# Kernel tuning notes

Hardware: AMD Instinct MI355X
Metric: run time of the kernel (lower is better)

## Reference

```python
import jax, jax.numpy as jnp
import numpy as np

B, S, D, H = 2, 2048, 1024, 16
DH = D // H  # dim_per_head = 64


def setup_inputs() -> dict:
    key = jax.random.key(0)
    ks = jax.random.split(key, 12)
    scale = 1.0 / np.sqrt(D)
    inp = {
        "key": jax.random.normal(ks[0], (B, S, D), jnp.float32),
        "value": jax.random.normal(ks[1], (B, S, D), jnp.float32),
        "query": jax.random.normal(ks[2], (B, S, D), jnp.float32),
        "mask": jax.random.randint(ks[3], (B, S, S), 0, 2) == 1,
        "Wq": jax.random.normal(ks[4], (D, D), jnp.float32) * scale,
        "bq": jnp.zeros((D,), jnp.float32),
        "Wk": jax.random.normal(ks[5], (D, D), jnp.float32) * scale,
        "bk": jnp.zeros((D,), jnp.float32),
        "Wv": jax.random.normal(ks[6], (D, D), jnp.float32) * scale,
        "bv": jnp.zeros((D,), jnp.float32),
        "Wo": jax.random.normal(ks[7], (D, D), jnp.float32) * scale,
        "bo": jnp.zeros((D,), jnp.float32),
    }
    return inp


def reference(key, value, query, mask, Wq, bq, Wk, bk, Wv, bv, Wo, bo):
    b, s, d = query.shape
    dh = d // H

    def split_heads(x):  # [b, s, d] -> [b, H, s, dh]
        return x.reshape(b, -1, H, dh).transpose(0, 2, 1, 3)

    q = split_heads(query @ Wq + bq) / jnp.sqrt(jnp.float32(dh))
    k = split_heads(key @ Wk + bk)
    v = split_heads(value @ Wv + bv)

    scores = jnp.einsum("bhqd,bhkd->bhqk", q, k)  # [b, H, s, s]
    scores = jnp.where(mask[:, None, :, :], jnp.float32(-1e18), scores)
    attn = jax.nn.softmax(scores, axis=-1)  # dropout is identity in eval
    ctx = jnp.einsum("bhqk,bhkd->bhqd", attn, v)
    ctx = ctx.transpose(0, 2, 1, 3).reshape(b, s, d)
    return ctx @ Wo + bo
```

## Files before the change

kernel.cpp:

```cpp
#include <hip/hip_runtime.h>
#include <hip/hip_bf16.h>

#define BATCH  2
#define SEQ    2048
#define DMODEL 1024
#define NHEAD  16
#define DHEAD  64
#define NTOK   (BATCH * SEQ)

using f32x4 = __attribute__((ext_vector_type(4))) float;
using s16x4 = __attribute__((ext_vector_type(4))) short;
using s16x8 = __attribute__((ext_vector_type(8))) short;

__device__ __forceinline__ short f2bf(float f) {
  __hip_bfloat16 h = __float2bfloat16(f);
  return *(short*)&h;
}

__device__ __forceinline__ void gload_lds16(const short* g, short* l) {
  __builtin_amdgcn_global_load_lds(
      (const __attribute__((address_space(1))) void*)g,
      (__attribute__((address_space(3))) void*)l, 16, 0, 0);
}

__global__ __launch_bounds__(256) void wtrans_kernel(
    const float* __restrict__ Wq, const float* __restrict__ Wk,
    const float* __restrict__ Wv, const float* __restrict__ Wo,
    short* __restrict__ Wt) {
  __shared__ short tile[64][72];
  const float* W = blockIdx.z == 0 ? Wq : blockIdx.z == 1 ? Wk
                 : blockIdx.z == 2 ? Wv : Wo;
  short* out = Wt + (size_t)blockIdx.z * DMODEL * DMODEL;
  int k0 = blockIdx.x * 64, n0 = blockIdx.y * 64;
  int t = threadIdx.x;
#pragma unroll
  for (int i = 0; i < 4; ++i) {
    int idx = t + i * 256;
    int row = idx >> 4, c4 = idx & 15;
    f32x4 v = *(const f32x4*)(W + (size_t)(k0 + row) * DMODEL + n0 + c4 * 4);
    s16x4 p;
    p[0] = f2bf(v[0]); p[1] = f2bf(v[1]); p[2] = f2bf(v[2]); p[3] = f2bf(v[3]);
    *(s16x4*)&tile[row][c4 * 4] = p;
  }
  __syncthreads();
#pragma unroll
  for (int i = 0; i < 2; ++i) {
    int idx = t + i * 256;
    int nrow = idx >> 3, c8 = idx & 7;
    s16x8 p;
#pragma unroll
    for (int j = 0; j < 8; ++j) p[j] = tile[c8 * 8 + j][nrow];
    *(s16x8*)(out + (size_t)(n0 + nrow) * DMODEL + k0 + c8 * 8) = p;
  }
}

__global__ __launch_bounds__(256) void mpack_kernel(
    const int* __restrict__ mask, unsigned long long* __restrict__ Mp) {
  const int total_words = BATCH * SEQ * (SEQ / 64);
  int lane = threadIdx.x & 63;
  int wv = blockIdx.x * 4 + (threadIdx.x >> 6);
  int nw = gridDim.x * 4;
  for (int w = wv; w < total_words; w += nw) {
    int mv = mask[(size_t)w * 64 + lane];
    unsigned long long bits = __ballot(mv != 0);
    if (lane == 0) Mp[w] = bits;
  }
}

__global__ __launch_bounds__(256) void proj_qkv_kernel(
    const float* __restrict__ Xq, const float* __restrict__ Xk,
    const float* __restrict__ Xv, const short* __restrict__ Wt,
    const float* __restrict__ bq, const float* __restrict__ bk,
    const float* __restrict__ bv, short* __restrict__ QKV) {
  __shared__ short As[2][128 * 32];
  __shared__ short Bs[2][128 * 32];
  const int sel = blockIdx.z;
  const float* X    = sel == 0 ? Xq : sel == 1 ? Xk : Xv;
  const float* bias = sel == 0 ? bq : sel == 1 ? bk : bv;
  const short* Wsel = Wt + (size_t)sel * DMODEL * DMODEL;
  short* Obuf = QKV + (size_t)sel * ((size_t)BATCH * NHEAD * SEQ * DHEAD);
  const float scale = sel == 0 ? 0.18033688011111793f : 1.0f;

  int m0 = blockIdx.x * 128, n0 = blockIdx.y * 128;
  int t = threadIdx.x, wid = t >> 6, lane = t & 63;
  int lr = lane & 15, lg = lane >> 4;
  int wr = wid >> 1, wc = wid & 1;
  f32x4 acc[4][4] = {};

  const int ar0 = t >> 2, ac0 = (t & 3) << 3;
  const float* Arow0 = X + (size_t)(m0 + ar0) * DMODEL + ac0;
  const float* Arow1 = Arow0 + (size_t)64 * DMODEL;
  const int aofs0 = ar0 * 32 + ac0, aofs1 = aofs0 + 64 * 32;
  const short* Brow0 = Wsel + (size_t)(n0 + ar0) * DMODEL + ac0;
  const short* Brow1 = Brow0 + (size_t)64 * DMODEL;
  const int bofs0 = (t & ~63) << 3, bofs1 = bofs0 + 256 * 8;

  f32x4 a00, a01, a10, a11;
#define LOADA(k0s) {                                                          \
    a00 = *(const f32x4*)(Arow0 + (k0s));                                     \
    a01 = *(const f32x4*)(Arow0 + (k0s) + 4);                                 \
    a10 = *(const f32x4*)(Arow1 + (k0s));                                     \
    a11 = *(const f32x4*)(Arow1 + (k0s) + 4); }
#define STAGEB(bufi, k0s) {                                                   \
    gload_lds16(Brow0 + (k0s), &Bs[bufi][0] + bofs0);                         \
    gload_lds16(Brow1 + (k0s), &Bs[bufi][0] + bofs1); }
#define WRITEA(bufi) {                                                        \
    s16x8 p0, p1;                                                             \
    p0[0]=f2bf(a00[0]); p0[1]=f2bf(a00[1]); p0[2]=f2bf(a00[2]); p0[3]=f2bf(a00[3]); \
    p0[4]=f2bf(a01[0]); p0[5]=f2bf(a01[1]); p0[6]=f2bf(a01[2]); p0[7]=f2bf(a01[3]); \
    p1[0]=f2bf(a10[0]); p1[1]=f2bf(a10[1]); p1[2]=f2bf(a10[2]); p1[3]=f2bf(a10[3]); \
    p1[4]=f2bf(a11[0]); p1[5]=f2bf(a11[1]); p1[6]=f2bf(a11[2]); p1[7]=f2bf(a11[3]); \
    *(s16x8*)(&As[bufi][0] + aofs0) = p0;                                     \
    *(s16x8*)(&As[bufi][0] + aofs1) = p1; }

  LOADA(0); STAGEB(0, 0); WRITEA(0);
  __syncthreads();

  int cur = 0;
  for (int kt = 0; kt < DMODEL / 32; ++kt) {
    if (kt + 1 < DMODEL / 32) {
      LOADA((kt + 1) * 32);
      STAGEB(cur ^ 1, (kt + 1) * 32);
    }
    s16x8 afr[4], bfr[4];
#pragma unroll
    for (int mi = 0; mi < 4; ++mi)
      afr[mi] = *(const s16x8*)(&As[cur][0] + (wr * 64 + mi * 16 + lr) * 32 + lg * 8);
#pragma unroll
    for (int ni = 0; ni < 4; ++ni)
      bfr[ni] = *(const s16x8*)(&Bs[cur][0] + (wc * 64 + ni * 16 + lr) * 32 + lg * 8);
    __builtin_amdgcn_s_setprio(1);
#pragma unroll
    for (int mi = 0; mi < 4; ++mi)
#pragma unroll
      for (int ni = 0; ni < 4; ++ni)
        acc[mi][ni] = __builtin_amdgcn_mfma_f32_16x16x32_bf16(
            afr[mi], bfr[ni], acc[mi][ni], 0, 0, 0);
    __builtin_amdgcn_s_setprio(0);
    if (kt + 1 < DMODEL / 32) WRITEA(cur ^ 1);
    __syncthreads();
    cur ^= 1;
  }
#undef LOADA
#undef STAGEB
#undef WRITEA

  if (sel == 2) {
    int bq_ = m0 >> 11;
    int s0 = (m0 & (SEQ - 1)) + wr * 64 + lg * 4;
#pragma unroll
    for (int mi = 0; mi < 4; ++mi)
#pragma unroll
      for (int ni = 0; ni < 4; ++ni) {
        int n = n0 + wc * 64 + ni * 16 + lr;
        float bv_ = bias[n];
        int h = n >> 6, d = n & 63;
        s16x4 pk;
#pragma unroll
        for (int r = 0; r < 4; ++r) pk[r] = f2bf(acc[mi][ni][r] + bv_);
        *(s16x4*)&Obuf[((size_t)(bq_ * NHEAD + h) * DHEAD + d) * SEQ
                       + s0 + mi * 16] = pk;
      }
  } else {
#pragma unroll
    for (int mi = 0; mi < 4; ++mi)
#pragma unroll
      for (int ni = 0; ni < 4; ++ni) {
        int n = n0 + wc * 64 + ni * 16 + lr;
        float bv_ = bias[n];
        int h = n >> 6, d = n & 63;
#pragma unroll
        for (int r = 0; r < 4; ++r) {
          int m = m0 + wr * 64 + mi * 16 + lg * 4 + r;
          int b = m >> 11, s = m & (SEQ - 1);
          float val = (acc[mi][ni][r] + bv_) * scale;
          Obuf[((size_t)(b * NHEAD + h) * SEQ + s) * DHEAD + d] = f2bf(val);
        }
      }
  }
}

__global__ __launch_bounds__(256) void attn_kernel(
    const short* __restrict__ Qb, const short* __restrict__ Kb,
    const short* __restrict__ VbT, const unsigned long long* __restrict__ Mp,
    short* __restrict__ Ctx) {
  __shared__ short Ks[2][64 * 64];
  __shared__ short Vt[2][64 * 64];
  __shared__ short Ps[4 * 16 * 64];
  int qt = blockIdx.x, bh = blockIdx.y;
  int b = bh >> 4, h = bh & 15;
  int q0 = qt * 64;
  int t = threadIdx.x, wid = t >> 6, lane = t & 63;
  int lr = lane & 15, lg = lane >> 4;
  int lr7 = lr & 7;

  const short* Qrow = Qb + ((size_t)bh * SEQ + q0 + wid * 16 + lr) * DHEAD;
  s16x8 qf[2];
  qf[0] = *(const s16x8*)(Qrow + lg * 8);
  qf[1] = *(const s16x8*)(Qrow + 32 + lg * 8);

  const short* KbB = Kb + (size_t)bh * SEQ * DHEAD;
  const short* VtB = VbT + (size_t)bh * DHEAD * SEQ;

  const int srow = lane >> 3;
  const int schunk = ((lane & 7) ^ srow) * 8;

  float m_run = -1e30f, l_run = 0.f;
  f32x4 o_acc[4] = {};

  const unsigned long long* mrow =
      Mp + ((size_t)b * SEQ + q0 + wid * 16 + lr) * (SEQ / 64);

#define STAGE(bufi, k0s)                                                      \
  {                                                                           \
    _Pragma("unroll")                                                         \
    for (int i = 0; i < 2; ++i) {                                             \
      int rbase = wid * 16 + i * 8;                                           \
      gload_lds16(KbB + (size_t)((k0s) + rbase + srow) * DHEAD + schunk,      \
                  &Ks[bufi][rbase * 64]);                                     \
      gload_lds16(VtB + (size_t)(rbase + srow) * SEQ + (k0s) + schunk,        \
                  &Vt[bufi][rbase * 64]);                                     \
    }                                                                         \
  }

  unsigned long long mw_cur = mrow[0];
  STAGE(0, 0);
  asm volatile("s_waitcnt vmcnt(0)" ::: "memory");
  __syncthreads();

  int cur = 0;
  for (int kt = 0; kt < SEQ / 64; ++kt) {
    unsigned long long mw_next = 0;
    if (kt + 1 < SEQ / 64) {
      STAGE(cur ^ 1, (kt + 1) * 64);
      mw_next = mrow[kt + 1];
    }
    const short* KsC = Ks[cur];
    const short* VtC = Vt[cur];

    f32x4 sfr[4];
    __builtin_amdgcn_s_setprio(1);
#pragma unroll
    for (int nf = 0; nf < 4; ++nf) {
      int row = nf * 16 + lr;
      s16x8 kf0 = *(const s16x8*)&KsC[row * 64 + ((lg ^ lr7) << 3)];
      s16x8 kf1 = *(const s16x8*)&KsC[row * 64 + (((4 + lg) ^ lr7) << 3)];
      f32x4 c = {};
      c = __builtin_amdgcn_mfma_f32_16x16x32_bf16(kf0, qf[0], c, 0, 0, 0);
      c = __builtin_amdgcn_mfma_f32_16x16x32_bf16(kf1, qf[1], c, 0, 0, 0);
      sfr[nf] = c;
    }
    __builtin_amdgcn_s_setprio(0);

    unsigned w0 = (unsigned)(mw_cur >> (lg * 4));
    unsigned w1 = (unsigned)(mw_cur >> (lg * 4 + 32));
#pragma unroll
    for (int nf = 0; nf < 4; ++nf)
#pragma unroll
      for (int r = 0; r < 4; ++r) {
        unsigned bit = (nf < 2) ? (w0 >> (nf * 16 + r)) : (w1 >> ((nf - 2) * 16 + r));
        if (bit & 1u) sfr[nf][r] = -1e30f;
      }
    float tm = fmaxf(fmaxf(fmaxf(sfr[0][0], sfr[0][1]), fmaxf(sfr[0][2], sfr[0][3])),
                     fmaxf(fmaxf(sfr[1][0], sfr[1][1]), fmaxf(sfr[1][2], sfr[1][3])));
    float tm2 = fmaxf(fmaxf(fmaxf(sfr[2][0], sfr[2][1]), fmaxf(sfr[2][2], sfr[2][3])),
                      fmaxf(fmaxf(sfr[3][0], sfr[3][1]), fmaxf(sfr[3][2], sfr[3][3])));
    tm = fmaxf(tm, tm2);
    tm = fmaxf(tm, __shfl_xor(tm, 16, 64));
    tm = fmaxf(tm, __shfl_xor(tm, 32, 64));

    bool small = __all(tm <= m_run + 8.0f);
    if (!small) {
      float mnew = fmaxf(m_run, tm);
      float scl = __builtin_amdgcn_exp2f(m_run - mnew);
      m_run = mnew;
      l_run *= scl;
      float scl_o[4];
#pragma unroll
      for (int r = 0; r < 4; ++r) scl_o[r] = __shfl(scl, lg * 4 + r, 64);
#pragma unroll
      for (int nf = 0; nf < 4; ++nf)
#pragma unroll
        for (int r = 0; r < 4; ++r) o_acc[nf][r] *= scl_o[r];
    }
    float ps4[4];
#pragma unroll
    for (int nf = 0; nf < 4; ++nf) {
#pragma unroll
      for (int r = 0; r < 4; ++r)
        sfr[nf][r] = __builtin_amdgcn_exp2f(sfr[nf][r] - m_run);
      ps4[nf] = (sfr[nf][0] + sfr[nf][1]) + (sfr[nf][2] + sfr[nf][3]);
    }
    float ps = (ps4[0] + ps4[1]) + (ps4[2] + ps4[3]);
    ps += __shfl_xor(ps, 16, 64);
    ps += __shfl_xor(ps, 32, 64);
    l_run += ps;

    int psbase = wid * (16 * 64) + lr * 64;
#pragma unroll
    for (int nf = 0; nf < 4; ++nf) {
      s16x4 pk;
#pragma unroll
      for (int r = 0; r < 4; ++r) pk[r] = f2bf(sfr[nf][r]);
      *(s16x4*)&Ps[psbase + ((((2 * nf + (lg >> 1)) ^ lr7) << 3) | ((lg & 1) << 2))] = pk;
    }
    asm volatile("s_waitcnt lgkmcnt(0)" ::: "memory");
    __builtin_amdgcn_sched_barrier(0);

    __builtin_amdgcn_s_setprio(1);
#pragma unroll
    for (int ks = 0; ks < 2; ++ks) {
      s16x8 pf = *(const s16x8*)&Ps[psbase + (((ks * 4 + lg) ^ lr7) << 3)];
#pragma unroll
      for (int nf = 0; nf < 4; ++nf) {
        int d = nf * 16 + lr;
        s16x8 vf = *(const s16x8*)&VtC[d * 64 + (((ks * 4 + lg) ^ lr7) << 3)];
        o_acc[nf] = __builtin_amdgcn_mfma_f32_16x16x32_bf16(pf, vf, o_acc[nf], 0, 0, 0);
      }
    }
    __builtin_amdgcn_s_setprio(0);

    asm volatile("s_waitcnt vmcnt(0)" ::: "memory");
    __syncthreads();
    cur ^= 1;
    mw_cur = mw_next;
  }
#undef STAGE
  float l_o[4];
#pragma unroll
  for (int r = 0; r < 4; ++r) l_o[r] = __shfl(l_run, lg * 4 + r, 64);
#pragma unroll
  for (int nf = 0; nf < 4; ++nf)
#pragma unroll
    for (int r = 0; r < 4; ++r) {
      int srow_ = q0 + wid * 16 + lg * 4 + r;
      float val = o_acc[nf][r] / l_o[r];
      Ctx[((size_t)b * SEQ + srow_) * DMODEL + h * DHEAD + nf * 16 + lr] = f2bf(val);
    }
}

__global__ __launch_bounds__(256) void proj_out_kernel(
    const short* __restrict__ Ctx, const short* __restrict__ Wot,
    const float* __restrict__ bo, float* __restrict__ Out) {
  __shared__ short As[2][128 * 32];
  __shared__ short Bs[2][128 * 32];
  int m0 = blockIdx.x * 128, n0 = blockIdx.y * 128;
  int t = threadIdx.x, wid = t >> 6, lane = t & 63;
  int lr = lane & 15, lg = lane >> 4;
  int wr = wid >> 1, wc = wid & 1;
  f32x4 acc[4][4] = {};

  const int gr0 = t >> 2, gc0 = (t & 3) << 3;
  const short* Actx0 = Ctx + (size_t)(m0 + gr0) * DMODEL + gc0;
  const short* Actx1 = Actx0 + (size_t)64 * DMODEL;
  const short* Bwo0 = Wot + (size_t)(n0 + gr0) * DMODEL + gc0;
  const short* Bwo1 = Bwo0 + (size_t)64 * DMODEL;
  const int lofs0 = (t & ~63) << 3, lofs1 = lofs0 + 256 * 8;

#define STAGE_PO(bufi, k0s) {                                                 \
    gload_lds16(Actx0 + (k0s), &As[bufi][0] + lofs0);                         \
    gload_lds16(Actx1 + (k0s), &As[bufi][0] + lofs1);                         \
    gload_lds16(Bwo0 + (k0s), &Bs[bufi][0] + lofs0);                          \
    gload_lds16(Bwo1 + (k0s), &Bs[bufi][0] + lofs1); }

  STAGE_PO(0, 0);
  __syncthreads();

  int cur = 0;
  for (int kt = 0; kt < DMODEL / 32; ++kt) {
    if (kt + 1 < DMODEL / 32) STAGE_PO(cur ^ 1, (kt + 1) * 32);
    s16x8 afr[4], bfr[4];
#pragma unroll
    for (int mi = 0; mi < 4; ++mi)
      afr[mi] = *(const s16x8*)(&As[cur][0] + (wr * 64 + mi * 16 + lr) * 32 + lg * 8);
#pragma unroll
    for (int ni = 0; ni < 4; ++ni)
      bfr[ni] = *(const s16x8*)(&Bs[cur][0] + (wc * 64 + ni * 16 + lr) * 32 + lg * 8);
    __builtin_amdgcn_s_setprio(1);
#pragma unroll
    for (int mi = 0; mi < 4; ++mi)
#pragma unroll
      for (int ni = 0; ni < 4; ++ni)
        acc[mi][ni] = __builtin_amdgcn_mfma_f32_16x16x32_bf16(
            afr[mi], bfr[ni], acc[mi][ni], 0, 0, 0);
    __builtin_amdgcn_s_setprio(0);
    __syncthreads();
    cur ^= 1;
  }
#undef STAGE_PO

#pragma unroll
  for (int mi = 0; mi < 4; ++mi)
#pragma unroll
    for (int ni = 0; ni < 4; ++ni) {
      int n = n0 + wc * 64 + ni * 16 + lr;
      float bv_ = bo[n];
#pragma unroll
      for (int r = 0; r < 4; ++r) {
        int m = m0 + wr * 64 + mi * 16 + lg * 4 + r;
        Out[(size_t)m * DMODEL + n] = acc[mi][ni][r] + bv_;
      }
    }
}

extern "C" void kernel_launch(void* const* d_in, const int* in_sizes, int n_in,
                              void* d_out, int out_size, void* d_ws, size_t ws_size,
                              hipStream_t stream) {
  const float* key_in   = (const float*)d_in[0];
  const float* value_in = (const float*)d_in[1];
  const float* query_in = (const float*)d_in[2];
  const int*   mask     = (const int*)d_in[3];
  const float* Wq = (const float*)d_in[4];
  const float* bq = (const float*)d_in[5];
  const float* Wk = (const float*)d_in[6];
  const float* bk = (const float*)d_in[7];
  const float* Wv = (const float*)d_in[8];
  const float* bv = (const float*)d_in[9];
  const float* Wo = (const float*)d_in[10];
  const float* bo = (const float*)d_in[11];
  float* out = (float*)d_out;

  short* ws = (short*)d_ws;
  const size_t WSZ   = (size_t)DMODEL * DMODEL;
  const size_t QKVSZ = (size_t)BATCH * NHEAD * SEQ * DHEAD;
  short* Wt  = ws;
  short* QKV = ws + 4 * WSZ;
  short* Qb  = QKV;
  short* Kb  = QKV + QKVSZ;
  short* VbT = QKV + 2 * QKVSZ;
  short* Ctx = QKV + 3 * QKVSZ;
  unsigned long long* Mp = (unsigned long long*)ws;

  wtrans_kernel<<<dim3(16, 16, 4), 256, 0, stream>>>(Wq, Wk, Wv, Wo, Wt);
  proj_qkv_kernel<<<dim3(32, 8, 3), 256, 0, stream>>>(
      query_in, key_in, value_in, Wt, bq, bk, bv, QKV);
  mpack_kernel<<<dim3(1024), 256, 0, stream>>>(mask, Mp);
  attn_kernel<<<dim3(32, 32), 256, 0, stream>>>(Qb, Kb, VbT, Mp, Ctx);
  proj_out_kernel<<<dim3(32, 8), 256, 0, stream>>>(Ctx, Wt + 3 * WSZ, bo, out);
}
```

Baseline: 190.5 us.

## Pre-cast activations to bf16 and remap grids for XCD-aware block placement

Adds a separate cast kernel that converts query/key/value to bf16 once, so the QKV projection can stage both operands with direct global-to-LDS loads instead of loading fp32 through registers and converting in the inner loop. It also flattens the grids of the projection, attention and output kernels and remaps block indices so consecutive blocks on the same XCD share tiles, aiming for better L2 reuse. The cost is an extra kernel launch plus an extra write and read of the bf16 activations. Ctx now aliases the Xb buffer, which is safe only because the QKV projection finishes before attention writes Ctx.

After: 189.0 us. No clear change (-0.8%).

```diff
diff --git a/kernel.cpp b/kernel.cpp
--- a/kernel.cpp
+++ b/kernel.cpp
@@ -54,6 +54,20 @@
   }
 }
 
+__global__ __launch_bounds__(256) void xcast_kernel(
+    const float* __restrict__ Xq, const float* __restrict__ Xk,
+    const float* __restrict__ Xv, short* __restrict__ Xb) {
+  int sel = blockIdx.y;
+  const float* src = sel == 0 ? Xq : sel == 1 ? Xk : Xv;
+  size_t off = ((size_t)blockIdx.x * 256 + threadIdx.x) * 8;
+  f32x4 v0 = *(const f32x4*)(src + off);
+  f32x4 v1 = *(const f32x4*)(src + off + 4);
+  s16x8 p;
+  p[0] = f2bf(v0[0]); p[1] = f2bf(v0[1]); p[2] = f2bf(v0[2]); p[3] = f2bf(v0[3]);
+  p[4] = f2bf(v1[0]); p[5] = f2bf(v1[1]); p[6] = f2bf(v1[2]); p[7] = f2bf(v1[3]);
+  *(s16x8*)(Xb + (size_t)sel * NTOK * DMODEL + off) = p;
+}
+
 __global__ __launch_bounds__(256) void mpack_kernel(
     const int* __restrict__ mask, unsigned long long* __restrict__ Mp) {
   const int total_words = BATCH * SEQ * (SEQ / 64);
@@ -68,60 +82,48 @@
 }
 
 __global__ __launch_bounds__(256) void proj_qkv_kernel(
-    const float* __restrict__ Xq, const float* __restrict__ Xk,
-    const float* __restrict__ Xv, const short* __restrict__ Wt,
+    const short* __restrict__ Xb, const short* __restrict__ Wt,
     const float* __restrict__ bq, const float* __restrict__ bk,
     const float* __restrict__ bv, short* __restrict__ QKV) {
   __shared__ short As[2][128 * 32];
   __shared__ short Bs[2][128 * 32];
-  const int sel = blockIdx.z;
-  const float* X    = sel == 0 ? Xq : sel == 1 ? Xk : Xv;
+  int wg = blockIdx.x;
+  int orig = (wg & 7) * 96 + (wg >> 3);
+  int sel = orig >> 8;
+  int rem = orig & 255;
+  int mx = rem >> 3, ny = rem & 7;
+
+  const short* X    = Xb + (size_t)sel * NTOK * DMODEL;
   const float* bias = sel == 0 ? bq : sel == 1 ? bk : bv;
   const short* Wsel = Wt + (size_t)sel * DMODEL * DMODEL;
   short* Obuf = QKV + (size_t)sel * ((size_t)BATCH * NHEAD * SEQ * DHEAD);
   const float scale = sel == 0 ? 0.18033688011111793f : 1.0f;
 
-  int m0 = blockIdx.x * 128, n0 = blockIdx.y * 128;
+  int m0 = mx * 128, n0 = ny * 128;
   int t = threadIdx.x, wid = t >> 6, lane = t & 63;
   int lr = lane & 15, lg = lane >> 4;
   int wr = wid >> 1, wc = wid & 1;
   f32x4 acc[4][4] = {};
 
-  const int ar0 = t >> 2, ac0 = (t & 3) << 3;
-  const float* Arow0 = X + (size_t)(m0 + ar0) * DMODEL + ac0;
-  const float* Arow1 = Arow0 + (size_t)64 * DMODEL;
-  const int aofs0 = ar0 * 32 + ac0, aofs1 = aofs0 + 64 * 32;
-  const short* Brow0 = Wsel + (size_t)(n0 + ar0) * DMODEL + ac0;
-  const short* Brow1 = Brow0 + (size_t)64 * DMODEL;
-  const int bofs0 = (t & ~63) << 3, bofs1 = bofs0 + 256 * 8;
-
-  f32x4 a00, a01, a10, a11;
-#define LOADA(k0s) {                                                          \
-    a00 = *(const f32x4*)(Arow0 + (k0s));                                     \
-    a01 = *(const f32x4*)(Arow0 + (k0s) + 4);                                 \
-    a10 = *(const f32x4*)(Arow1 + (k0s));                                     \
-    a11 = *(const f32x4*)(Arow1 + (k0s) + 4); }
-#define STAGEB(bufi, k0s) {                                                   \
-    gload_lds16(Brow0 + (k0s), &Bs[bufi][0] + bofs0);                         \
-    gload_lds16(Brow1 + (k0s), &Bs[bufi][0] + bofs1); }
-#define WRITEA(bufi) {                                                        \
-    s16x8 p0, p1;                                                             \
-    p0[0]=f2bf(a00[0]); p0[1]=f2bf(a00[1]); p0[2]=f2bf(a00[2]); p0[3]=f2bf(a00[3]); \
-    p0[4]=f2bf(a01[0]); p0[5]=f2bf(a01[1]); p0[6]=f2bf(a01[2]); p0[7]=f2bf(a01[3]); \
-    p1[0]=f2bf(a10[0]); p1[1]=f2bf(a10[1]); p1[2]=f2bf(a10[2]); p1[3]=f2bf(a10[3]); \
-    p1[4]=f2bf(a11[0]); p1[5]=f2bf(a11[1]); p1[6]=f2bf(a11[2]); p1[7]=f2bf(a11[3]); \
-    *(s16x8*)(&As[bufi][0] + aofs0) = p0;                                     \
-    *(s16x8*)(&As[bufi][0] + aofs1) = p1; }
-
-  LOADA(0); STAGEB(0, 0); WRITEA(0);
+  const int gr0 = t >> 2, gc0 = (t & 3) << 3;
+  const short* Ax0 = X + (size_t)(m0 + gr0) * DMODEL + gc0;
+  const short* Ax1 = Ax0 + (size_t)64 * DMODEL;
+  const short* Bw0 = Wsel + (size_t)(n0 + gr0) * DMODEL + gc0;
+  const short* Bw1 = Bw0 + (size_t)64 * DMODEL;
+  const int lofs0 = (t & ~63) << 3, lofs1 = lofs0 + 256 * 8;
+
+#define STAGEQ(bufi, k0s) {                                                   \
+    gload_lds16(Ax0 + (k0s), &As[bufi][0] + lofs0);                           \
+    gload_lds16(Ax1 + (k0s), &As[bufi][0] + lofs1);                           \
+    gload_lds16(Bw0 + (k0s), &Bs[bufi][0] + lofs0);                           \
+    gload_lds16(Bw1 + (k0s), &Bs[bufi][0] + lofs1); }
+
+  STAGEQ(0, 0);
   __syncthreads();
 
   int cur = 0;
   for (int kt = 0; kt < DMODEL / 32; ++kt) {
-    if (kt + 1 < DMODEL / 32) {
-      LOADA((kt + 1) * 32);
-      STAGEB(cur ^ 1, (kt + 1) * 32);
-    }
+    if (kt + 1 < DMODEL / 32) STAGEQ(cur ^ 1, (kt + 1) * 32);
     s16x8 afr[4], bfr[4];
 #pragma unroll
     for (int mi = 0; mi < 4; ++mi)
@@ -137,13 +139,10 @@
         acc[mi][ni] = __builtin_amdgcn_mfma_f32_16x16x32_bf16(
             afr[mi], bfr[ni], acc[mi][ni], 0, 0, 0);
     __builtin_amdgcn_s_setprio(0);
-    if (kt + 1 < DMODEL / 32) WRITEA(cur ^ 1);
     __syncthreads();
     cur ^= 1;
   }
-#undef LOADA
-#undef STAGEB
-#undef WRITEA
+#undef STAGEQ
 
   if (sel == 2) {
     int bq_ = m0 >> 11;
@@ -187,7 +186,9 @@
   __shared__ short Ks[2][64 * 64];
   __shared__ short Vt[2][64 * 64];
   __shared__ short Ps[4 * 16 * 64];
-  int qt = blockIdx.x, bh = blockIdx.y;
+  int wg = blockIdx.x;
+  int orig = (wg & 7) * 128 + (wg >> 3);
+  int bh = orig >> 5, qt = orig & 31;
   int b = bh >> 4, h = bh & 15;
   int q0 = qt * 64;
   int t = threadIdx.x, wid = t >> 6, lane = t & 63;
@@ -344,7 +345,10 @@
     const float* __restrict__ bo, float* __restrict__ Out) {
   __shared__ short As[2][128 * 32];
   __shared__ short Bs[2][128 * 32];
-  int m0 = blockIdx.x * 128, n0 = blockIdx.y * 128;
+  int wg = blockIdx.x;
+  int orig = (wg & 7) * 32 + (wg >> 3);
+  int mx = orig >> 3, ny = orig & 7;
+  int m0 = mx * 128, n0 = ny * 128;
   int t = threadIdx.x, wid = t >> 6, lane = t & 63;
   int lr = lane & 15, lg = lane >> 4;
   int wr = wid >> 1, wc = wid & 1;
@@ -423,18 +427,20 @@
   short* ws = (short*)d_ws;
   const size_t WSZ   = (size_t)DMODEL * DMODEL;
   const size_t QKVSZ = (size_t)BATCH * NHEAD * SEQ * DHEAD;
+  const size_t XSZ   = (size_t)NTOK * DMODEL;
   short* Wt  = ws;
   short* QKV = ws + 4 * WSZ;
   short* Qb  = QKV;
   short* Kb  = QKV + QKVSZ;
   short* VbT = QKV + 2 * QKVSZ;
-  short* Ctx = QKV + 3 * QKVSZ;
+  short* Xb  = ws + 4 * WSZ + 3 * QKVSZ;
+  short* Ctx = Xb;
   unsigned long long* Mp = (unsigned long long*)ws;
 
   wtrans_kernel<<<dim3(16, 16, 4), 256, 0, stream>>>(Wq, Wk, Wv, Wo, Wt);
-  proj_qkv_kernel<<<dim3(32, 8, 3), 256, 0, stream>>>(
-      query_in, key_in, value_in, Wt, bq, bk, bv, QKV);
+  xcast_kernel<<<dim3(2048, 3), 256, 0, stream>>>(query_in, key_in, value_in, Xb);
+  proj_qkv_kernel<<<dim3(768), 256, 0, stream>>>(Xb, Wt, bq, bk, bv, QKV);
   mpack_kernel<<<dim3(1024), 256, 0, stream>>>(mask, Mp);
-  attn_kernel<<<dim3(32, 32), 256, 0, stream>>>(Qb, Kb, VbT, Mp, Ctx);
-  proj_out_kernel<<<dim3(32, 8), 256, 0, stream>>>(Ctx, Wt + 3 * WSZ, bo, out);
-}
+  attn_kernel<<<dim3(1024), 256, 0, stream>>>(Qb, Kb, VbT, Mp, Ctx);
+  proj_out_kernel<<<dim3(256), 256, 0, stream>>>(Ctx, Wt + 3 * WSZ, bo, out);
+}
```
